# Performance work log

Hardware: AMD Instinct MI355X
Metric: run time of the kernel (lower is better)

The kernel has to match this reference:

```python
import jax, jax.numpy as jnp
import numpy as np

B, L, E, H, NL = 2, 1024, 1024, 16, 3
D = E // H
SCALE = D ** -0.5
EPS = 1e-5


def rmsnorm(x, g):
    return x * jax.lax.rsqrt(jnp.mean(x * x, axis=-1, keepdims=True) + EPS) * g


def rope(x, cos, sin):
    # x: (B, m*L, H, D); cos/sin: (L, D). Tile cos/sin to the growing KV length
    # (the source broadcasts rel_pos over the concatenated cache).
    m = x.shape[1] // cos.shape[0]
    c = jnp.tile(cos, (m, 1))[None, :, None, :]
    s = jnp.tile(sin, (m, 1))[None, :, None, :]
    x1, x2 = jnp.split(x, 2, axis=-1)
    rot = jnp.concatenate([-x2, x1], axis=-1)  # rotate_half convention
    return x * c + rot * s


def setup_inputs() -> dict:
    key = jax.random.key(0)
    ks = jax.random.split(key, 8)
    x = jax.random.normal(ks[0], (B, L, E), jnp.float32)
    inv_freq = 1.0 / (10000.0 ** (jnp.arange(0, D, 2, dtype=jnp.float32) / D))
    t = jnp.arange(L, dtype=jnp.float32)[:, None] * inv_freq[None, :]  # (L, D/2)
    cos = jnp.concatenate([jnp.cos(t), jnp.cos(t)], axis=-1)
    sin = jnp.concatenate([jnp.sin(t), jnp.sin(t)], axis=-1)
    attn_mask = jnp.where(jnp.tril(jnp.ones((L, L), bool)), 0.0, -jnp.inf).astype(jnp.float32)
    w_scale = E ** -0.5  # ~kaiming_uniform fan_in magnitude
    Wq = jax.random.normal(ks[1], (NL, E, E), jnp.float32) * w_scale
    Wk = jax.random.normal(ks[2], (NL, E, E), jnp.float32) * w_scale
    Wv = jax.random.normal(ks[3], (NL, E, E), jnp.float32) * w_scale
    Wo = jax.random.normal(ks[4], (E, E), jnp.float32) * w_scale
    lambdas = jax.random.normal(ks[5], (NL,), jnp.float32)
    g_ln = jnp.ones((NL, E), jnp.float32)
    g_final = jnp.ones((E,), jnp.float32)
    alpha = jnp.ones((1,), jnp.float32)
    return dict(x=x, cos=cos, sin=sin, attn_mask=attn_mask, Wq=Wq, Wk=Wk, Wv=Wv,
                g_ln=g_ln, lambdas=lambdas, Wo=Wo, g_final=g_final, alpha=alpha)


def reference(x, cos, sin, attn_mask, Wq, Wk, Wv, g_ln, lambdas, Wo, g_final, alpha):
    # lambda weights: sigmoid then non-affine LayerNorm across the NL layers
    s = jax.nn.sigmoid(lambdas)
    lw = (s - s.mean()) * jax.lax.rsqrt(s.var() + EPS)

    acc_k, acc_v = [], []
    outs = []
    for i in range(NL):
        q = (x @ Wq[i].T).reshape(B, L, H, D)
        k = (x @ Wk[i].T).reshape(B, L, H, D)
        v = (x @ Wv[i].T).reshape(B, L, H, D)
        if i > 0:  # prepend-current growing KV cache (source concatenates [k, accumulated])
            k = jnp.concatenate([k] + acc_k, axis=1)
            v = jnp.concatenate([v] + acc_v, axis=1)
        q = rope(q, cos, sin)
        k = rope(k, cos, sin)
        KV = k.shape[1]
        scores = jnp.einsum('bqhd,bkhd->bhqk', q * SCALE, k)  # (B,H,L,KV)
        if i == 0:
            m = attn_mask
        else:  # source fills everything past tgt_len with -inf
            m = jnp.concatenate(
                [attn_mask, jnp.full((L, KV - L), -jnp.inf, attn_mask.dtype)], axis=1)
        w = jax.nn.softmax(scores + m, axis=-1)
        a = jnp.einsum('bhqk,bkhd->bqhd', w, v).reshape(B, L, E)
        outs.append(rmsnorm(a, g_ln[i]) * lw[i])
        acc_k.append(k)  # stores the full concatenated, roped k (lengths 1L,2L,4L)
        acc_v.append(v)
    combined = outs[0] + outs[1] + outs[2]
    out = rmsnorm(combined + alpha * x, g_final)
    return out @ Wo.T
```

## Files before the change

### kernel.cpp

```cpp
#include <hip/hip_runtime.h>


#define B_  2
#define L_  1024
#define E_  1024
#define H_  16
#define NL_ 3
#define D_  64

typedef __bf16 bf16_t;
typedef __bf16 bf16x8 __attribute__((ext_vector_type(8)));
typedef __bf16 bf16x4 __attribute__((ext_vector_type(4)));
typedef float  f32x4  __attribute__((ext_vector_type(4)));

#define NEG_INF (-__builtin_inff())

typedef const __attribute__((address_space(1))) void* gas_ptr;
typedef __attribute__((address_space(3))) void* las_ptr;

#define GLD_LDS16(gp, lp) \
  __builtin_amdgcn_global_load_lds((gas_ptr)(gp), (las_ptr)(lp), 16, 0, 0)

__global__ __launch_bounds__(256) void cvt_k(
    const float* __restrict__ s0, const float* __restrict__ s1,
    const float* __restrict__ s2, const float* __restrict__ s3,
    const float* __restrict__ s4, bf16_t* __restrict__ d0,
    bf16_t* __restrict__ d1, bf16_t* __restrict__ d2, bf16_t* __restrict__ d3,
    bf16_t* __restrict__ d4)
{
  const int seg = blockIdx.y;
  const float* s;
  bf16_t* d;
  int n;
  if (seg == 0)      { s = s0; d = d0; n = 3145728; }
  else if (seg == 1) { s = s1; d = d1; n = 3145728; }
  else if (seg == 2) { s = s2; d = d2; n = 3145728; }
  else if (seg == 3) { s = s3; d = d3; n = 1048576; }
  else               { s = s4; d = d4; n = 2097152; }
  const int i = (blockIdx.x * 256 + threadIdx.x) * 4;
  if (i < n) {
    const float4 v = *(const float4*)(s + i);
    bf16x4 o;
    o[0] = (bf16_t)v.x; o[1] = (bf16_t)v.y; o[2] = (bf16_t)v.z; o[3] = (bf16_t)v.w;
    *(bf16x4*)(d + i) = o;
  }
}

template <int EPI>
__global__ __launch_bounds__(256) void gemm_k(
    const bf16_t* __restrict__ X, const bf16_t* __restrict__ W0,
    const bf16_t* __restrict__ W1, const bf16_t* __restrict__ W2,
    const float* __restrict__ cosb, const float* __restrict__ sinb,
    bf16_t* __restrict__ qk, bf16_t* __restrict__ vt, float* __restrict__ outf)
{
  __shared__ bf16_t smem[16384];
  const int tid = threadIdx.x;
  const int lane = tid & 63;
  const int w = tid >> 6;
  const int q4 = lane >> 4, l15 = lane & 15;
  const int row0swz = (l15 >> 1) & 3;

  const int flat0 = blockIdx.y * 16 + blockIdx.x;
  const int chunk = (EPI ? 128 : 1152) >> 3;
  const int nf = (flat0 & 7) * chunk + (flat0 >> 3);
  const int bxs = nf & 15;
  const int bys = nf >> 4;

  const int row0 = bxs * 128;

  int g, tileN;
  const bf16_t* Wb;
  if (EPI == 0) {
    g = bys >> 3;
    tileN = bys & 7;
    const int t = g % 3, il = g / 3;
    Wb = (t == 0 ? W0 : (t == 1 ? W1 : W2)) + (size_t)il * E_ * E_;
  } else {
    g = 0;
    tileN = bys;
    Wb = W0;
  }
  const int col0 = tileN * 128;
  const int rA = (w & 1) * 64;
  const int cB = (w >> 1) * 64;

  const int srow = tid >> 2;
  const int sgcol = (((tid & 3) ^ ((tid >> 3) & 3)) << 3);

  f32x4 acc[4][4] = {};

  const size_t xrow = (size_t)(row0 + srow) * E_ + sgcol;
  const size_t xrow2 = xrow + (size_t)64 * E_;
  const size_t wrow = (size_t)(col0 + srow) * E_ + sgcol;
  const size_t wrow2 = wrow + (size_t)64 * E_;

#define STAGE_(buf, st)                                          \
  do {                                                           \
    bf16_t* Xb = smem + (buf) * 8192;                            \
    bf16_t* Wbl = smem + (buf) * 8192 + 4096;                    \
    const int k0_ = (st) * 32;                                   \
    GLD_LDS16(X + xrow + k0_, &Xb[tid * 8]);                     \
    GLD_LDS16(X + xrow2 + k0_, &Xb[2048 + tid * 8]);             \
    GLD_LDS16(Wb + wrow + k0_, &Wbl[tid * 8]);                   \
    GLD_LDS16(Wb + wrow2 + k0_, &Wbl[2048 + tid * 8]);           \
  } while (0)

#define COMPUTE_(buf)                                            \
  do {                                                           \
    const bf16_t* Xb = smem + (buf) * 8192;                      \
    const bf16_t* Wbl = smem + (buf) * 8192 + 4096;              \
    bf16x8 a[4], b[4];                                           \
    const int slot = (q4 ^ row0swz) << 3;                        \
    _Pragma("unroll")                                            \
    for (int mi = 0; mi < 4; ++mi)                               \
      a[mi] = *(const bf16x8*)&Xb[(rA + mi * 16 + l15) * 32 + slot]; \
    _Pragma("unroll")                                            \
    for (int ni = 0; ni < 4; ++ni)                               \
      b[ni] = *(const bf16x8*)&Wbl[(cB + ni * 16 + l15) * 32 + slot]; \
    _Pragma("unroll")                                            \
    for (int mi = 0; mi < 4; ++mi)                               \
      _Pragma("unroll")                                          \
      for (int ni = 0; ni < 4; ++ni)                             \
        acc[mi][ni] = __builtin_amdgcn_mfma_f32_16x16x32_bf16(   \
            a[mi], b[ni], acc[mi][ni], 0, 0, 0);                 \
  } while (0)

  STAGE_(0, 0);
#pragma unroll 1
  for (int t = 0; t < 31; ++t) {
    STAGE_((t + 1) & 1, t + 1);
    asm volatile("s_waitcnt vmcnt(4)\n\ts_barrier" ::: "memory");
    COMPUTE_(t & 1);
    asm volatile("s_barrier" ::: "memory");
  }
  asm volatile("s_waitcnt vmcnt(0)\n\ts_barrier" ::: "memory");
  COMPUTE_(1);

#undef STAGE_
#undef COMPUTE_

  if (EPI == 0) {
    const int t = g % 3, il = g / 3;
    if (t < 2) {
      const int slot = il * 2 + t;
      const int h = tileN * 2 + (w >> 1);
      const float post = (t == 0) ? 0.18033688011112042f : 1.0f;
#pragma unroll
      for (int mi = 0; mi < 4; ++mi) {
#pragma unroll
        for (int reg = 0; reg < 4; ++reg) {
          const int m = row0 + rA + mi * 16 + q4 * 4 + reg;
          const int b = m >> 10, l = m & (L_ - 1);
#pragma unroll
          for (int ni = 0; ni < 4; ++ni) {
            const int d = ni * 16 + l15;
            const float v0 = acc[mi][ni][reg];
            const float part = acc[mi][ni ^ 2][reg];
            const float rot = (d < 32) ? -part : part;
            const float v = (v0 * cosb[l * D_ + d] + rot * sinb[l * D_ + d]) * post;
            qk[(((size_t)slot * B_ + b) * H_ + h) * ((size_t)L_ * D_) +
               (size_t)l * D_ + d] = (bf16_t)v;
          }
        }
      }
    } else {
      const int n_l = tid >> 1, lh = tid & 1;
      const int h = tileN * 2 + (n_l >> 6), d = n_l & 63;
      const int bb = row0 >> 10;
      __syncthreads();
#pragma unroll
      for (int p = 0; p < 2; ++p) {
        if ((w & 1) == p) {
#pragma unroll
          for (int mi = 0; mi < 4; ++mi)
#pragma unroll
            for (int reg = 0; reg < 4; ++reg)
#pragma unroll
              for (int ni = 0; ni < 4; ++ni)
                smem[(cB + ni * 16 + l15) * 72 + mi * 16 + q4 * 4 + reg] =
                    (bf16_t)acc[mi][ni][reg];
        }
        __syncthreads();
        const int l0 = (row0 & (L_ - 1)) + p * 64 + lh * 32;
        bf16_t* gp = vt + (((size_t)il * B_ + bb) * H_ + h) * ((size_t)D_ * L_) +
                     (size_t)d * L_ + l0;
        const bf16_t* sp = &smem[n_l * 72 + lh * 32];
#pragma unroll
        for (int c = 0; c < 4; ++c)
          *(bf16x8*)(gp + c * 8) = *(const bf16x8*)(sp + c * 8);
        if (p == 0) __syncthreads();
      }
    }
  } else {
#pragma unroll
    for (int mi = 0; mi < 4; ++mi) {
#pragma unroll
      for (int reg = 0; reg < 4; ++reg) {
        const int m = row0 + rA + mi * 16 + q4 * 4 + reg;
#pragma unroll
        for (int ni = 0; ni < 4; ++ni) {
          const int n = col0 + cB + ni * 16 + l15;
          outf[(size_t)m * E_ + n] = acc[mi][ni][reg];
        }
      }
    }
  }
}

__global__ __launch_bounds__(256) void attn_k(const bf16_t* __restrict__ qk,
                                              const bf16_t* __restrict__ vt,
                                              bf16_t* __restrict__ attn)
{
  __shared__ bf16_t Ks[2][64 * 64];
  __shared__ bf16_t Vts[2][64 * 64];
  __shared__ bf16_t Ps[4][16 * 72];

  const int tid = threadIdx.x, lane = tid & 63, w = tid >> 6;
  const int q4 = lane >> 4, l15 = lane & 15;

  const int flat0 = blockIdx.y * 8 + blockIdx.x;
  const int nf = (flat0 & 7) * 96 + (flat0 >> 3);
  const int x = nf & 7;
  const int by = nf >> 3;

  const int h = by & 15, b = (by >> 4) & 1, i = by >> 5;
  const size_t HD = (size_t)L_ * D_;
  const bf16_t* Qp = qk + (((size_t)(i * 2 + 0) * B_ + b) * H_ + h) * HD;
  const bf16_t* Kp = qk + (((size_t)(i * 2 + 1) * B_ + b) * H_ + h) * HD;
  const bf16_t* Vp = vt + (((size_t)i * B_ + b) * H_ + h) * HD;

  const int srow = tid >> 3;
  const int sg = tid & 7;
  const int scol = (sg ^ (srow & 7)) * 8;

  bf16x8 ones;
#pragma unroll
  for (int jj = 0; jj < 8; ++jj) ones[jj] = (bf16_t)1.0f;

#pragma unroll 1
  for (int ph = 0; ph < 2; ++ph) {
    const int qt = ph == 0 ? (15 - x) : x;

    bf16x8 aq[2];
#pragma unroll
    for (int kk = 0; kk < 2; ++kk)
      aq[kk] = *(const bf16x8*)(Qp + (size_t)(qt * 64 + w * 16 + l15) * 64 +
                                kk * 32 + q4 * 8);

    if (ph == 1) __syncthreads();
#pragma unroll
    for (int it = 0; it < 2; ++it) {
      const int flat = it * 2048 + tid * 8;
      const int r = it * 32 + srow;
      GLD_LDS16(Kp + r * 64 + scol, &Ks[0][flat]);
      GLD_LDS16(Vp + (size_t)r * L_ + scol, &Vts[0][flat]);
    }

    f32x4 o[4] = {};
    f32x4 lacc = {};

#pragma unroll 1
    for (int j = 0; j <= qt; ++j) {
      __syncthreads();
      const int cur = j & 1;
      if (j < qt) {
        const int nxt = cur ^ 1;
#pragma unroll
        for (int it = 0; it < 2; ++it) {
          const int flat = it * 2048 + tid * 8;
          const int r = it * 32 + srow;
          GLD_LDS16(Kp + (j + 1) * 4096 + r * 64 + scol, &Ks[nxt][flat]);
          GLD_LDS16(Vp + (size_t)r * L_ + (j + 1) * 64 + scol, &Vts[nxt][flat]);
        }
      }

      f32x4 s[4] = {};
#pragma unroll
      for (int kk = 0; kk < 2; ++kk) {
#pragma unroll
        for (int ni = 0; ni < 4; ++ni) {
          const bf16x8 bk =
              *(const bf16x8*)&Ks[cur][(ni * 16 + l15) * 64 +
                                       (((kk * 4 + q4) ^ (l15 & 7)) << 3)];
          s[ni] = __builtin_amdgcn_mfma_f32_16x16x32_bf16(aq[kk], bk, s[ni], 0, 0, 0);
        }
      }

      if (j == qt) {
#pragma unroll
        for (int reg = 0; reg < 4; ++reg)
#pragma unroll
          for (int ni = 0; ni < 4; ++ni)
            if (ni * 16 + l15 > w * 16 + q4 * 4 + reg) s[ni][reg] = NEG_INF;
      }

#pragma unroll
      for (int reg = 0; reg < 4; ++reg)
#pragma unroll
        for (int ni = 0; ni < 4; ++ni)
          Ps[w][(q4 * 4 + reg) * 72 + ni * 16 + l15] = (bf16_t)exp2f(s[ni][reg]);
      asm volatile("s_waitcnt lgkmcnt(0)" ::: "memory");

#pragma unroll
      for (int kk = 0; kk < 2; ++kk) {
        const bf16x8 ap = *(const bf16x8*)&Ps[w][l15 * 72 + kk * 32 + q4 * 8];
        lacc = __builtin_amdgcn_mfma_f32_16x16x32_bf16(ap, ones, lacc, 0, 0, 0);
#pragma unroll
        for (int di = 0; di < 4; ++di) {
          const bf16x8 bv =
              *(const bf16x8*)&Vts[cur][(di * 16 + l15) * 64 +
                                        (((kk * 4 + q4) ^ (l15 & 7)) << 3)];
          o[di] = __builtin_amdgcn_mfma_f32_16x16x32_bf16(ap, bv, o[di], 0, 0, 0);
        }
      }
    }

    const int row_base = (i * B_ + b) * L_ + qt * 64 + w * 16 + q4 * 4;
#pragma unroll
    for (int reg = 0; reg < 4; ++reg) {
      const float inv = 1.f / lacc[reg];
      const int r = row_base + reg;
#pragma unroll
      for (int di = 0; di < 4; ++di)
        attn[(size_t)r * E_ + h * 64 + di * 16 + l15] = (bf16_t)(o[di][reg] * inv);
    }
  }
}

__device__ __forceinline__ float block_sum(float v, float* sm)
{
#pragma unroll
  for (int off = 32; off > 0; off >>= 1) v += __shfl_xor(v, off);
  const int w = threadIdx.x >> 6;
  __syncthreads();
  if ((threadIdx.x & 63) == 0) sm[w] = v;
  __syncthreads();
  return sm[0] + sm[1] + sm[2] + sm[3];
}

__global__ __launch_bounds__(256) void combine_k(
    const bf16_t* __restrict__ attn, const float* __restrict__ x,
    const float* __restrict__ g_ln, const float* __restrict__ lambdas,
    const float* __restrict__ g_final, const float* __restrict__ alphap,
    bf16_t* __restrict__ xn)
{
  __shared__ float sm[4];
  const int row = blockIdx.x;
  const int tid = threadIdx.x;

  float sg[3], lw[3];
#pragma unroll
  for (int i = 0; i < 3; ++i) sg[i] = 1.f / (1.f + expf(-lambdas[i]));
  const float mean = (sg[0] + sg[1] + sg[2]) * (1.f / 3.f);
  const float var = ((sg[0] - mean) * (sg[0] - mean) + (sg[1] - mean) * (sg[1] - mean) +
                     (sg[2] - mean) * (sg[2] - mean)) * (1.f / 3.f);
  const float rv = rsqrtf(var + 1e-5f);
#pragma unroll
  for (int i = 0; i < 3; ++i) lw[i] = (sg[i] - mean) * rv;

  const float av = alphap[0];
  float c[4];
#pragma unroll
  for (int k = 0; k < 4; ++k) {
    const int e = tid + k * 256;
    c[k] = av * x[(size_t)row * E_ + e];
  }

  for (int i = 0; i < 3; ++i) {
    float a[4];
    float ss = 0.f;
#pragma unroll
    for (int k = 0; k < 4; ++k) {
      const int e = tid + k * 256;
      a[k] = (float)attn[((size_t)i * (B_ * L_) + row) * E_ + e];
      ss += a[k] * a[k];
    }
    ss = block_sum(ss, sm);
    const float rinv = rsqrtf(ss * (1.f / (float)E_) + 1e-5f);
#pragma unroll
    for (int k = 0; k < 4; ++k) {
      const int e = tid + k * 256;
      c[k] += a[k] * rinv * g_ln[i * E_ + e] * lw[i];
    }
  }

  float ss = 0.f;
#pragma unroll
  for (int k = 0; k < 4; ++k) ss += c[k] * c[k];
  ss = block_sum(ss, sm);
  const float rinv = rsqrtf(ss * (1.f / (float)E_) + 1e-5f);
#pragma unroll
  for (int k = 0; k < 4; ++k) {
    const int e = tid + k * 256;
    xn[(size_t)row * E_ + e] = (bf16_t)(c[k] * rinv * g_final[e]);
  }
}

extern "C" void kernel_launch(void* const* d_in, const int* in_sizes, int n_in,
                              void* d_out, int out_size, void* d_ws, size_t ws_size,
                              hipStream_t stream)
{
  const float* x       = (const float*)d_in[0];
  const float* cosb    = (const float*)d_in[1];
  const float* sinb    = (const float*)d_in[2];
  const float* Wq      = (const float*)d_in[4];
  const float* Wk      = (const float*)d_in[5];
  const float* Wv      = (const float*)d_in[6];
  const float* g_ln    = (const float*)d_in[7];
  const float* lambdas = (const float*)d_in[8];
  const float* Wo      = (const float*)d_in[9];
  const float* g_final = (const float*)d_in[10];
  const float* alphap  = (const float*)d_in[11];

  bf16_t* qk    = (bf16_t*)d_ws;
  bf16_t* VT    = (bf16_t*)((char*)d_ws + 25165824);
  bf16_t* attnb = (bf16_t*)((char*)d_ws + 37748736);
  bf16_t* Wqb   = (bf16_t*)((char*)d_ws + 50331648);
  bf16_t* Wkb   = Wqb + 3145728;
  bf16_t* Wvb   = Wkb + 3145728;
  bf16_t* Wob   = (bf16_t*)((char*)d_ws + 69206016);
  bf16_t* xb    = (bf16_t*)((char*)d_ws + 71303168);
  bf16_t* xnb   = (bf16_t*)d_ws;
  float*  out   = (float*)d_out;

  cvt_k<<<dim3(3072, 5), 256, 0, stream>>>(Wq, Wk, Wv, Wo, x, Wqb, Wkb, Wvb, Wob, xb);
  gemm_k<0><<<dim3(16, 72), 256, 0, stream>>>(xb, Wqb, Wkb, Wvb, cosb, sinb,
                                              qk, VT, nullptr);
  attn_k<<<dim3(8, 96), 256, 0, stream>>>(qk, VT, attnb);
  combine_k<<<dim3(B_ * L_), 256, 0, stream>>>(attnb, x, g_ln, lambdas, g_final,
                                               alphap, xnb);
  gemm_k<1><<<dim3(16, 8), 256, 0, stream>>>(xnb, Wob, Wob, Wob, cosb, sinb,
                                             nullptr, nullptr, out);
}
```

Measured before the change: 229.1 us.

## Restructure attention to 32x32 MFMA with register-resident P and merged query tiles

```diff
diff --git a/kernel.cpp b/kernel.cpp
--- a/kernel.cpp
+++ b/kernel.cpp
@@ -12,6 +12,8 @@
 typedef __bf16 bf16x8 __attribute__((ext_vector_type(8)));
 typedef __bf16 bf16x4 __attribute__((ext_vector_type(4)));
 typedef float  f32x4  __attribute__((ext_vector_type(4)));
+typedef float  f32x16 __attribute__((ext_vector_type(16)));
+typedef int    i32x2  __attribute__((ext_vector_type(2)));
 
 #define NEG_INF (-__builtin_inff())
 
@@ -213,10 +215,10 @@
 {
   __shared__ bf16_t Ks[2][64 * 64];
   __shared__ bf16_t Vts[2][64 * 64];
-  __shared__ bf16_t Ps[4][16 * 72];
 
   const int tid = threadIdx.x, lane = tid & 63, w = tid >> 6;
-  const int q4 = lane >> 4, l15 = lane & 15;
+  const int l31 = lane & 31, hi = lane >> 5;
+  const bool hib = (hi != 0);
 
   const int flat0 = blockIdx.y * 8 + blockIdx.x;
   const int nf = (flat0 & 7) * 96 + (flat0 >> 3);
@@ -233,98 +235,122 @@
   const int sg = tid & 7;
   const int scol = (sg ^ (srow & 7)) * 8;
 
-  bf16x8 ones;
-#pragma unroll
-  for (int jj = 0; jj < 8; ++jj) ones[jj] = (bf16_t)1.0f;
+  const int qta = 15 - x;
+  const int qtw = (w < 2) ? qta : x;
+  const int qw  = w & 1;
+
+  bf16x8 aq[4];
+  const size_t qoff = (size_t)(qtw * 64 + qw * 32 + l31) * 64 + hi * 8;
+#pragma unroll
+  for (int ks = 0; ks < 4; ++ks)
+    aq[ks] = *(const bf16x8*)(Qp + qoff + ks * 16);
+
+#pragma unroll
+  for (int it = 0; it < 2; ++it) {
+    const int flat = it * 2048 + tid * 8;
+    const int r = it * 32 + srow;
+    GLD_LDS16(Kp + r * 64 + scol, &Ks[0][flat]);
+    GLD_LDS16(Vp + (size_t)r * L_ + scol, &Vts[0][flat]);
+  }
+
+  f32x16 o[2] = {};
+  float psum = 0.f;
 
 #pragma unroll 1
-  for (int ph = 0; ph < 2; ++ph) {
-    const int qt = ph == 0 ? (15 - x) : x;
-
-    bf16x8 aq[2];
-#pragma unroll
-    for (int kk = 0; kk < 2; ++kk)
-      aq[kk] = *(const bf16x8*)(Qp + (size_t)(qt * 64 + w * 16 + l15) * 64 +
-                                kk * 32 + q4 * 8);
-
-    if (ph == 1) __syncthreads();
-#pragma unroll
-    for (int it = 0; it < 2; ++it) {
-      const int flat = it * 2048 + tid * 8;
-      const int r = it * 32 + srow;
-      GLD_LDS16(Kp + r * 64 + scol, &Ks[0][flat]);
-      GLD_LDS16(Vp + (size_t)r * L_ + scol, &Vts[0][flat]);
-    }
-
-    f32x4 o[4] = {};
-    f32x4 lacc = {};
-
-#pragma unroll 1
-    for (int j = 0; j <= qt; ++j) {
-      __syncthreads();
-      const int cur = j & 1;
-      if (j < qt) {
-        const int nxt = cur ^ 1;
-#pragma unroll
-        for (int it = 0; it < 2; ++it) {
-          const int flat = it * 2048 + tid * 8;
-          const int r = it * 32 + srow;
-          GLD_LDS16(Kp + (j + 1) * 4096 + r * 64 + scol, &Ks[nxt][flat]);
-          GLD_LDS16(Vp + (size_t)r * L_ + (j + 1) * 64 + scol, &Vts[nxt][flat]);
-        }
-      }
-
-      f32x4 s[4] = {};
-#pragma unroll
-      for (int kk = 0; kk < 2; ++kk) {
-#pragma unroll
-        for (int ni = 0; ni < 4; ++ni) {
-          const bf16x8 bk =
-              *(const bf16x8*)&Ks[cur][(ni * 16 + l15) * 64 +
-                                       (((kk * 4 + q4) ^ (l15 & 7)) << 3)];
-          s[ni] = __builtin_amdgcn_mfma_f32_16x16x32_bf16(aq[kk], bk, s[ni], 0, 0, 0);
-        }
-      }
-
-      if (j == qt) {
-#pragma unroll
-        for (int reg = 0; reg < 4; ++reg)
-#pragma unroll
-          for (int ni = 0; ni < 4; ++ni)
-            if (ni * 16 + l15 > w * 16 + q4 * 4 + reg) s[ni][reg] = NEG_INF;
-      }
-
-#pragma unroll
-      for (int reg = 0; reg < 4; ++reg)
-#pragma unroll
-        for (int ni = 0; ni < 4; ++ni)
-          Ps[w][(q4 * 4 + reg) * 72 + ni * 16 + l15] = (bf16_t)exp2f(s[ni][reg]);
-      asm volatile("s_waitcnt lgkmcnt(0)" ::: "memory");
-
-#pragma unroll
-      for (int kk = 0; kk < 2; ++kk) {
-        const bf16x8 ap = *(const bf16x8*)&Ps[w][l15 * 72 + kk * 32 + q4 * 8];
-        lacc = __builtin_amdgcn_mfma_f32_16x16x32_bf16(ap, ones, lacc, 0, 0, 0);
-#pragma unroll
-        for (int di = 0; di < 4; ++di) {
-          const bf16x8 bv =
-              *(const bf16x8*)&Vts[cur][(di * 16 + l15) * 64 +
-                                        (((kk * 4 + q4) ^ (l15 & 7)) << 3)];
-          o[di] = __builtin_amdgcn_mfma_f32_16x16x32_bf16(ap, bv, o[di], 0, 0, 0);
-        }
-      }
-    }
-
-    const int row_base = (i * B_ + b) * L_ + qt * 64 + w * 16 + q4 * 4;
-#pragma unroll
-    for (int reg = 0; reg < 4; ++reg) {
-      const float inv = 1.f / lacc[reg];
-      const int r = row_base + reg;
-#pragma unroll
-      for (int di = 0; di < 4; ++di)
-        attn[(size_t)r * E_ + h * 64 + di * 16 + l15] = (bf16_t)(o[di][reg] * inv);
-    }
-  }
+  for (int j = 0; j <= qta; ++j) {
+    __syncthreads();
+    const int cur = j & 1;
+    if (j < qta) {
+      const int nxt = cur ^ 1;
+#pragma unroll
+      for (int it = 0; it < 2; ++it) {
+        const int flat = it * 2048 + tid * 8;
+        const int r = it * 32 + srow;
+        GLD_LDS16(Kp + (j + 1) * 4096 + r * 64 + scol, &Ks[nxt][flat]);
+        GLD_LDS16(Vp + (size_t)r * L_ + (j + 1) * 64 + scol, &Vts[nxt][flat]);
+      }
+    }
+    if (j <= qtw) {
+      f32x16 s[2] = {};
+#pragma unroll
+      for (int ks = 0; ks < 4; ++ks) {
+#pragma unroll
+        for (int kvb = 0; kvb < 2; ++kvb) {
+          const int r = kvb * 32 + l31;
+          const bf16x8 ak = *(const bf16x8*)&Ks[cur][r * 64 +
+                                ((((ks << 1) | hi) ^ (r & 7)) << 3)];
+          s[kvb] = __builtin_amdgcn_mfma_f32_32x32x16_bf16(ak, aq[ks], s[kvb],
+                                                           0, 0, 0);
+        }
+      }
+
+      if (j == qtw) {
+#pragma unroll
+        for (int kvb = 0; kvb < 2; ++kvb)
+#pragma unroll
+          for (int reg = 0; reg < 16; ++reg) {
+            const int kv = kvb * 32 + (reg & 3) + ((reg >> 2) << 3) + (hi << 2);
+            if (kv > qw * 32 + l31) s[kvb][reg] = NEG_INF;
+          }
+      }
+
+      bf16x4 oq[2][4];
+#pragma unroll
+      for (int kvb = 0; kvb < 2; ++kvb)
+#pragma unroll
+        for (int r2 = 0; r2 < 4; ++r2)
+#pragma unroll
+          for (int r3 = 0; r3 < 4; ++r3) {
+            const float pv = exp2f(s[kvb][(r2 << 2) | r3]);
+            psum += pv;
+            oq[kvb][r2][r3] = (bf16_t)pv;
+          }
+
+      bf16x4 swq[2][4];
+#pragma unroll
+      for (int kvb = 0; kvb < 2; ++kvb)
+#pragma unroll
+        for (int r2 = 0; r2 < 4; ++r2) {
+          const i32x2 v = *(const i32x2*)&oq[kvb][r2];
+          i32x2 t;
+          t[0] = __shfl_xor(v[0], 32);
+          t[1] = __shfl_xor(v[1], 32);
+          swq[kvb][r2] = *(const bf16x4*)&t;
+        }
+
+#pragma unroll
+      for (int ks2 = 0; ks2 < 4; ++ks2) {
+        const int kvb = ks2 >> 1, k1 = ks2 & 1;
+        const bf16x4 Fq = hib ? swq[kvb][2 * k1 + 1] : oq[kvb][2 * k1];
+        const bf16x4 Sq = hib ? oq[kvb][2 * k1 + 1] : swq[kvb][2 * k1];
+        bf16x8 bp;
+#pragma unroll
+        for (int e = 0; e < 4; ++e) { bp[e] = Fq[e]; bp[4 + e] = Sq[e]; }
+#pragma unroll
+        for (int db = 0; db < 2; ++db) {
+          const int rv = db * 32 + l31;
+          const bf16x8 av = *(const bf16x8*)&Vts[cur][rv * 64 +
+                                ((((ks2 << 1) | hi) ^ (rv & 7)) << 3)];
+          o[db] = __builtin_amdgcn_mfma_f32_32x32x16_bf16(av, bp, o[db],
+                                                          0, 0, 0);
+        }
+      }
+    }
+  }
+
+  const float inv = 1.f / (psum + __shfl_xor(psum, 32));
+  const int rq = (i * B_ + b) * L_ + qtw * 64 + qw * 32 + l31;
+  bf16_t* gp = attn + (size_t)rq * E_ + h * 64 + hi * 4;
+#pragma unroll
+  for (int db = 0; db < 2; ++db)
+#pragma unroll
+    for (int r2 = 0; r2 < 4; ++r2) {
+      bf16x4 ov;
+#pragma unroll
+      for (int r3 = 0; r3 < 4; ++r3)
+        ov[r3] = (bf16_t)(o[db][(r2 << 2) | r3] * inv);
+      *(bf16x4*)(gp + db * 32 + r2 * 8) = ov;
+    }
 }
 
 __device__ __forceinline__ float block_sum(float v, float* sm)
```

Result: slower. 241.6 us (+5.5%).
